# Kernel tuning notes

Hardware: AMD Instinct MI355X
Metric: run time of the kernel (lower is better)

Reference implementation:

```python
import jax, jax.numpy as jnp
import numpy as np

L, N, EMB, H = 4, 50000, 128, 4
R, HID, LBL = 16, 64, 32
E = 625000


def setup_inputs() -> dict:
    key = jax.random.key(0)
    ks = jax.random.split(key, 10)
    s = 0.05
    return {
        "embedding": jax.random.normal(ks[0], (L, N, EMB), jnp.float32),
        "in_proj_w": jax.random.normal(ks[1], (3 * EMB, EMB), jnp.float32) * s,
        "in_proj_b": jnp.zeros((3 * EMB,), jnp.float32),
        "out_proj_w": jax.random.normal(ks[2], (EMB, EMB), jnp.float32) * s,
        "out_proj_b": jnp.zeros((EMB,), jnp.float32),
        "w1": jax.random.normal(ks[3], (R, EMB, HID), jnp.float32) * s,
        "root1": jax.random.normal(ks[4], (EMB, HID), jnp.float32) * s,
        "b1": jnp.zeros((HID,), jnp.float32),
        "w2": jax.random.normal(ks[5], (R, HID, LBL), jnp.float32) * s,
        "root2": jax.random.normal(ks[6], (HID, LBL), jnp.float32) * s,
        "b2": jnp.zeros((LBL,), jnp.float32),
        "edge_index": jax.random.randint(ks[7], (2, E), 0, N, dtype=jnp.int64),
        "edge_type": jax.random.randint(ks[8], (E,), 0, R, dtype=jnp.int64),
    }


def mha_self(x, wi, bi, wo, bo):
    # x: (L, N, EMB) -- torch nn.MultiheadAttention, batch_first=False, q=k=v=x
    Ls, Ns, Es = x.shape
    hd = Es // H
    qkv = x @ wi.T + bi                      # (L, N, 3E)
    q, k, v = jnp.split(qkv, 3, axis=-1)
    q = q.reshape(Ls, Ns, H, hd)
    k = k.reshape(Ls, Ns, H, hd)
    v = v.reshape(Ls, Ns, H, hd)
    scores = jnp.einsum('lnhd,mnhd->nhlm', q, k) / np.sqrt(hd).astype(np.float32)
    attn = jax.nn.softmax(scores, axis=-1)
    out = jnp.einsum('nhlm,mnhd->lnhd', attn, v).reshape(Ls, Ns, Es)
    return out @ wo.T + bo


def rgcn_layer(x, src, dst, etype, W, root, bias):
    # PyG RGCNConv (num_bases=None, aggr='mean'):
    # out[n] = x[n] @ root + bias + sum_r mean_{e: dst=n, type=r} x[src_e] @ W[r]
    Rr, fin, fout = W.shape
    seg = etype * N + dst                                   # (E,) combined (rel, dst)
    msg_sum = jax.ops.segment_sum(x[src], seg, num_segments=Rr * N)   # (R*N, fin)
    cnt = jax.ops.segment_sum(jnp.ones((src.shape[0],), x.dtype), seg,
                              num_segments=Rr * N)
    mean = (msg_sum / jnp.maximum(cnt, 1.0)[:, None]).reshape(Rr, N, fin)
    agg = jnp.einsum('rni,rio->no', mean, W)                # per-relation GEMM
    return agg + x @ root + bias


def reference(embedding, in_proj_w, in_proj_b, out_proj_w, out_proj_b,
              w1, root1, b1, w2, root2, b2, edge_index, edge_type):
    attn_out = mha_self(embedding, in_proj_w, in_proj_b, out_proj_w, out_proj_b)
    x = attn_out[0]                                         # (N, EMB)
    src, dst = edge_index[0], edge_index[1]
    x = jax.nn.relu(rgcn_layer(x, src, dst, edge_type, w1, root1, b1))
    x = rgcn_layer(x, src, dst, edge_type, w2, root2, b2)
    return jax.nn.softmax(x, axis=-1)
```

## Files before the change

kernel.cpp:

```cpp
#include <hip/hip_runtime.h>
#include <hip/hip_bf16.h>
#include <math.h>

#define NNODES 50000
#define NEDGE 625000
#define RREL 16
#define SCAN_NB 196

typedef __attribute__((ext_vector_type(8))) short short8;
typedef __attribute__((ext_vector_type(4))) float f32x4;

__device__ __forceinline__ float bfu(ushort u) {
  return __uint_as_float(((unsigned)u) << 16);
}
__device__ __forceinline__ ushort f2b(float f) {
  __hip_bfloat16 h = __float2bfloat16(f);
  return *(ushort*)&h;
}

__global__ __launch_bounds__(256) void prep_weights(
    const float* __restrict__ ipw, const float* __restrict__ opw,
    const float* __restrict__ w1, const float* __restrict__ root1,
    const float* __restrict__ w2, const float* __restrict__ root2,
    __hip_bfloat16* __restrict__ BTqkv, __hip_bfloat16* __restrict__ BToutT,
    __hip_bfloat16* __restrict__ BT1, __hip_bfloat16* __restrict__ BT2) {
  int i = blockIdx.x * 256 + threadIdx.x;
  if (i < 49152) {
    BTqkv[i] = __float2bfloat16(ipw[i]);
  } else if (i < 65536) {
    int j = i - 49152; int m = j / 128, c = j % 128;
    BToutT[j] = __float2bfloat16(opw[c * 128 + m]);
  } else if (i < 65536 + 139264) {
    int j = i - 65536; int c = j / 128, k = j % 128;
    float v;
    if (c < 64) v = root1[k * 64 + c];
    else { int r = (c - 64) >> 6, o = (c - 64) & 63; v = w1[r * 8192 + k * 64 + o]; }
    BT1[j] = __float2bfloat16(v);
  } else if (i < 65536 + 139264 + 34816) {
    int j = i - 65536 - 139264; int c = j / 64, k = j % 64;
    float v;
    if (c < 32) v = root2[k * 32 + c];
    else { int r = (c - 32) >> 5, o = (c - 32) & 31; v = w2[r * 2048 + k * 32 + o]; }
    BT2[j] = __float2bfloat16(v);
  }
}

__global__ __launch_bounds__(256) void prep_bias1(
    const float* __restrict__ opb, const float* __restrict__ w1,
    const float* __restrict__ root1, float* __restrict__ bias1) {
  int j = blockIdx.x * 256 + threadIdx.x;
  if (j >= 1088) return;
  float s = 0.f;
  if (j < 64) {
    for (int c = 0; c < 128; c++) s += opb[c] * root1[c * 64 + j];
  } else {
    int r = (j - 64) >> 6, o = (j - 64) & 63;
    for (int c = 0; c < 128; c++) s += opb[c] * w1[r * 8192 + c * 64 + o];
  }
  bias1[j] = s;
}

__global__ __launch_bounds__(256) void qkv_gemm(
    const float* __restrict__ A, const __hip_bfloat16* __restrict__ BT,
    const float* __restrict__ bias, __hip_bfloat16* __restrict__ C) {
  __shared__ ushort As[128 * 128];
  __shared__ ushort Cs[128 * 136];
  const int t = threadIdx.x;
  const long row0 = (long)blockIdx.x * 128;

  {
    float4 fa[16];
#pragma unroll
    for (int it = 0; it < 8; it++) {
      int c = t + it * 256;
      int r = c >> 4, cc = c & 15;
      long gm = row0 + r; if (gm > 199999) gm = 199999;
      const float* ap = A + gm * 128 + cc * 8;
      fa[2 * it]     = *(const float4*)ap;
      fa[2 * it + 1] = *(const float4*)(ap + 4);
    }
#pragma unroll
    for (int it = 0; it < 8; it++) {
      int c = t + it * 256;
      int r = c >> 4, cc = c & 15;
      int4 v = make_int4(0, 0, 0, 0);
      if (row0 + r < 200000) {
        float4 f0 = fa[2 * it], f1 = fa[2 * it + 1];
        v.x = (int)f2b(f0.x) | ((int)f2b(f0.y) << 16);
        v.y = (int)f2b(f0.z) | ((int)f2b(f0.w) << 16);
        v.z = (int)f2b(f1.x) | ((int)f2b(f1.y) << 16);
        v.w = (int)f2b(f1.z) | ((int)f2b(f1.w) << 16);
      }
      *(int4*)(As + r * 128 + ((cc ^ (r & 7)) * 8)) = v;
    }
  }
  __syncthreads();

  const int lane = t & 63, w = t >> 6;
  const int wr = (w >> 1) * 64, wc = (w & 1) * 64;
  const int lrow = lane & 15, lk = lane >> 4;
  const int nstrips = (row0 < NNODES) ? 3 : 2;

  for (int s = 0; s < nstrips; s++) {
    const int col0 = (s == 2) ? 0 : 128 + s * 128;
    const long Meff = (s == 2) ? NNODES : 200000;

    const ushort* bp[4];
#pragma unroll
    for (int j = 0; j < 4; j++)
      bp[j] = (const ushort*)BT + (long)(col0 + wc + j * 16 + lrow) * 128 + lk * 8;

    short8 bfr[4][4];
#pragma unroll
    for (int k0 = 0; k0 < 4; k0++)
#pragma unroll
      for (int j = 0; j < 4; j++)
        bfr[k0][j] = *(const short8*)(bp[j] + k0 * 32);

    f32x4 acc[4][4];
#pragma unroll
    for (int i = 0; i < 4; i++)
#pragma unroll
      for (int j = 0; j < 4; j++) acc[i][j] = (f32x4){0.f, 0.f, 0.f, 0.f};

#pragma unroll
    for (int k0 = 0; k0 < 4; k0++) {
      const int cb = k0 * 4 + lk;
      short8 af[4];
#pragma unroll
      for (int i = 0; i < 4; i++) {
        int ra = wr + i * 16 + lrow;
        af[i] = *(const short8*)(As + ra * 128 + ((cb ^ (ra & 7)) * 8));
      }
#pragma unroll
      for (int i = 0; i < 4; i++)
#pragma unroll
        for (int j = 0; j < 4; j++)
          acc[i][j] = __builtin_amdgcn_mfma_f32_16x16x32_bf16(af[i], bfr[k0][j], acc[i][j], 0, 0, 0);
    }

    __syncthreads();
#pragma unroll
    for (int j = 0; j < 4; j++) {
      int coll = wc + j * 16 + lrow;
      float bv = bias[col0 + coll];
#pragma unroll
      for (int i = 0; i < 4; i++) {
        int rbase = wr + i * 16 + lk * 4;
#pragma unroll
        for (int q = 0; q < 4; q++)
          Cs[(rbase + q) * 136 + coll] = f2b(acc[i][j][q] + bv);
      }
    }
    __syncthreads();
#pragma unroll
    for (int idx = t; idx < 128 * 16; idx += 256) {
      int r = idx >> 4, k = idx & 15;
      long gm = row0 + r;
      if (gm < Meff)
        *(int4*)((ushort*)C + gm * 384 + col0 + k * 8) = *(const int4*)(Cs + r * 136 + k * 8);
    }
  }
}

#define EPILOGUE_STORE(MEFF, NCOLS, LDC, BIASEXPR)                              \
  for (int p = 0; p < 2; p++) {                                                 \
    __syncthreads();                                                            \
    if ((w >> 1) == p) {                                                        \
      _Pragma("unroll")                                                         \
      for (int j = 0; j < 4; j++) {                                             \
        int coll = wc + j * 16 + lrow;                                          \
        float bv = (BIASEXPR);                                                  \
        _Pragma("unroll")                                                       \
        for (int i = 0; i < 4; i++) {                                           \
          int rloc = i * 16 + lk * 4;                                           \
          _Pragma("unroll")                                                     \
          for (int q = 0; q < 4; q++)                                           \
            Cs[(rloc + q) * 132 + coll] = f2b(acc[i][j][q] + bv);               \
        }                                                                       \
      }                                                                         \
    }                                                                           \
    __syncthreads();                                                            \
    _Pragma("unroll")                                                           \
    for (int idx = t; idx < 64 * 16; idx += 256) {                              \
      int r = idx >> 4, k = idx & 15;                                           \
      long gm = row0 + p * 64 + r;                                              \
      int col = col0 + k * 8;                                                   \
      if (gm < (MEFF) && col < (NCOLS))                                         \
        *(int4*)((ushort*)C + gm * (LDC) + col) = *(const int4*)(Cs + r * 132 + k * 8); \
    }                                                                           \
  }

template <int K>
__global__ __launch_bounds__(256) void gemm_strips(
    const __hip_bfloat16* __restrict__ Av, const __hip_bfloat16* __restrict__ BT,
    const float* __restrict__ bias, __hip_bfloat16* __restrict__ C,
    int M, int N, int ldc, int spg) {
  constexpr int CPR = K / 8;
  constexpr int NIT = 128 * CPR / 256;
  constexpr int NK0 = K / 32;
  __shared__ ushort As[128 * K];
  __shared__ ushort Cs[64 * 132];
  const int t = threadIdx.x;
  const long row0 = (long)blockIdx.x * 128;

  {
    int4 st[NIT];
#pragma unroll
    for (int it = 0; it < NIT; it++) {
      int c = t + it * 256;
      int r = c / CPR, cc = c % CPR;
      long gm = row0 + r; if (gm > M - 1) gm = M - 1;
      st[it] = *(const int4*)((const ushort*)Av + gm * K + cc * 8);
    }
#pragma unroll
    for (int it = 0; it < NIT; it++) {
      int c = t + it * 256;
      int r = c / CPR, cc = c % CPR;
      int4 v = (row0 + r < M) ? st[it] : make_int4(0, 0, 0, 0);
      *(int4*)(As + r * K + ((cc ^ (r & 7)) * 8)) = v;
    }
  }
  __syncthreads();

  const int lane = t & 63, w = t >> 6;
  const int wr = (w >> 1) * 64, wc = (w & 1) * 64;
  const int lrow = lane & 15, lk = lane >> 4;
  const int nstrips = (N + 127) / 128;
  const int sbeg = blockIdx.y * spg;
  const int send = min(sbeg + spg, nstrips);

  for (int s = sbeg; s < send; s++) {
    const int col0 = s * 128;

    const ushort* bp[4];
#pragma unroll
    for (int j = 0; j < 4; j++) {
      int gn = col0 + wc + j * 16 + lrow;
      if (gn > N - 1) gn = N - 1;
      bp[j] = (const ushort*)BT + (long)gn * K + lk * 8;
    }

    short8 bfr[NK0][4];
#pragma unroll
    for (int k0 = 0; k0 < NK0; k0++)
#pragma unroll
      for (int j = 0; j < 4; j++)
        bfr[k0][j] = *(const short8*)(bp[j] + k0 * 32);

    f32x4 acc[4][4];
#pragma unroll
    for (int i = 0; i < 4; i++)
#pragma unroll
      for (int j = 0; j < 4; j++) acc[i][j] = (f32x4){0.f, 0.f, 0.f, 0.f};

#pragma unroll
    for (int k0 = 0; k0 < NK0; k0++) {
      const int cb = k0 * 4 + lk;
      short8 af[4];
#pragma unroll
      for (int i = 0; i < 4; i++) {
        int ra = wr + i * 16 + lrow;
        af[i] = *(const short8*)(As + ra * K + ((cb ^ (ra & 7)) * 8));
      }
#pragma unroll
      for (int i = 0; i < 4; i++)
#pragma unroll
        for (int j = 0; j < 4; j++)
          acc[i][j] = __builtin_amdgcn_mfma_f32_16x16x32_bf16(af[i], bfr[k0][j], acc[i][j], 0, 0, 0);
    }

    EPILOGUE_STORE(M, N, ldc, bias ? bias[min(col0 + coll, N - 1)] : 0.f)
  }
}

__global__ __launch_bounds__(256) void attn_kernel(
    const __hip_bfloat16* __restrict__ qkv, __hip_bfloat16* __restrict__ o0) {
  int w = threadIdx.x >> 6, lane = threadIdx.x & 63;
  int n = blockIdx.x * 4 + w;
  const ushort* base = (const ushort*)qkv;
  uint qv = *(const uint*)(base + (size_t)n * 384 + lane * 2);
  uint kk[4], vv[4];
#pragma unroll
  for (int m = 0; m < 4; m++) {
    kk[m] = *(const uint*)(base + (size_t)(m * NNODES + n) * 384 + 128 + lane * 2);
    vv[m] = *(const uint*)(base + (size_t)(m * NNODES + n) * 384 + 256 + lane * 2);
  }
  float q0 = bfu(qv & 0xffff), q1 = bfu(qv >> 16);
  float s[4];
#pragma unroll
  for (int m = 0; m < 4; m++) {
    float p = q0 * bfu(kk[m] & 0xffff) + q1 * bfu(kk[m] >> 16);
#pragma unroll
    for (int off = 8; off; off >>= 1) p += __shfl_xor(p, off);
    s[m] = p * 0.17677669529663687f;
  }
  float mx = fmaxf(fmaxf(s[0], s[1]), fmaxf(s[2], s[3]));
  float e[4], sum = 0.f;
#pragma unroll
  for (int m = 0; m < 4; m++) { e[m] = __expf(s[m] - mx); sum += e[m]; }
  float inv = 1.0f / sum;
  float o0f = 0.f, o1f = 0.f;
#pragma unroll
  for (int m = 0; m < 4; m++) {
    float wgt = e[m] * inv;
    o0f += wgt * bfu(vv[m] & 0xffff);
    o1f += wgt * bfu(vv[m] >> 16);
  }
  *(uint*)((ushort*)o0 + (size_t)n * 128 + lane * 2) = (uint)f2b(o0f) | ((uint)f2b(o1f) << 16);
}

__global__ __launch_bounds__(256) void count_edges(
    const int* __restrict__ dst, const int* __restrict__ et, int* __restrict__ cnt) {
  int e = blockIdx.x * 256 + threadIdx.x;
  if (e < NEDGE) atomicAdd(&cnt[et[e] * NNODES + dst[e]], 1);
}

__global__ __launch_bounds__(256) void scan1(
    const int* __restrict__ cnt, int* __restrict__ off, int* __restrict__ part) {
  int t = threadIdx.x, b = blockIdx.x;
  int i = b * 256 + t;
  int v = 0;
  if (i < NNODES) {
#pragma unroll
    for (int r = 0; r < RREL; r++) v += cnt[r * NNODES + i];
  }
  __shared__ int sm[256];
  sm[t] = v;
  __syncthreads();
#pragma unroll
  for (int o = 1; o < 256; o <<= 1) {
    int x = (t >= o) ? sm[t - o] : 0;
    __syncthreads();
    sm[t] += x;
    __syncthreads();
  }
  if (i < NNODES) off[i] = sm[t] - v;
  if (t == 255) part[b] = sm[t];
}

__global__ __launch_bounds__(256) void scan2(int* __restrict__ part) {
  int t = threadIdx.x;
  int v = (t < SCAN_NB) ? part[t] : 0;
  __shared__ int sm[256];
  sm[t] = v;
  __syncthreads();
#pragma unroll
  for (int o = 1; o < 256; o <<= 1) {
    int x = (t >= o) ? sm[t - o] : 0;
    __syncthreads();
    sm[t] += x;
    __syncthreads();
  }
  if (t < SCAN_NB) part[t] = sm[t] - v;
}

__global__ __launch_bounds__(256) void scan3(int* __restrict__ off, const int* __restrict__ part) {
  int i = blockIdx.x * 256 + threadIdx.x;
  if (i < NNODES) off[i] += part[blockIdx.x];
  if (i == 0) off[NNODES] = NEDGE;
}

__global__ __launch_bounds__(256) void scatter_edges(
    const int* __restrict__ src, const int* __restrict__ dst, const int* __restrict__ et,
    const int* __restrict__ cnt, const int* __restrict__ off,
    int* __restrict__ fill, unsigned* __restrict__ sorted, float* __restrict__ scales) {
  int e = blockIdx.x * 256 + threadIdx.x;
  if (e >= NEDGE) return;
  int d = dst[e], r = et[e], s = src[e];
  int pos = off[d] + atomicAdd(&fill[d], 1);
  sorted[pos] = (unsigned)s | ((unsigned)r << 16);
  scales[pos] = 1.0f / (float)cnt[r * NNODES + d];
}

__global__ __launch_bounds__(256) void fused1(
    const int* __restrict__ off, const unsigned* __restrict__ sorted,
    const float* __restrict__ scales, const ushort* __restrict__ Y1,
    const float* __restrict__ b1, __hip_bfloat16* __restrict__ x1b) {
  int w = threadIdx.x >> 6, lane = threadIdx.x & 63;
  int d = blockIdx.x * 4 + w;
  int s0 = off[d], s1 = off[d + 1];
  float a[8];
  a[0] = bfu(Y1[(size_t)d * 1088 + lane]) + b1[lane];
#pragma unroll
  for (int j = 1; j < 8; j++) a[j] = 0.f;
  int i = s0;
  for (; i + 7 < s1; i += 8) {
    unsigned p[8];
    float c[8];
#pragma unroll
    for (int j = 0; j < 8; j++) { p[j] = sorted[i + j]; c[j] = scales[i + j]; }
#pragma unroll
    for (int j = 0; j < 8; j++)
      a[j] += bfu(Y1[(size_t)(p[j] & 0xFFFF) * 1088 + 64 + (p[j] >> 16) * 64 + lane]) * c[j];
  }
  for (; i < s1; i++) {
    unsigned p = sorted[i];
    a[0] += bfu(Y1[(size_t)(p & 0xFFFF) * 1088 + 64 + (p >> 16) * 64 + lane]) * scales[i];
  }
  float acc = ((a[0] + a[1]) + (a[2] + a[3])) + ((a[4] + a[5]) + (a[6] + a[7]));
  x1b[(size_t)d * 64 + lane] = __float2bfloat16(fmaxf(acc, 0.f));
}

__global__ __launch_bounds__(256) void fused2(
    const int* __restrict__ off, const unsigned* __restrict__ sorted,
    const float* __restrict__ scales, const ushort* __restrict__ Y2,
    const float* __restrict__ b2, float* __restrict__ out) {
  int w = threadIdx.x >> 6, lane = threadIdx.x & 63;
  int d = blockIdx.x * 4 + w;
  int j = lane & 31, half = lane >> 5;
  int s0 = off[d], s1 = off[d + 1];
  float a0 = 0.f, a1 = 0.f, a2 = 0.f, a3 = 0.f;
  int i = s0 + half;
  for (; i + 6 < s1; i += 8) {
    unsigned p0 = sorted[i], p1 = sorted[i + 2], p2 = sorted[i + 4], p3 = sorted[i + 6];
    float c0 = scales[i], c1 = scales[i + 2], c2 = scales[i + 4], c3 = scales[i + 6];
    a0 += bfu(Y2[(size_t)(p0 & 0xFFFF) * 544 + 32 + (p0 >> 16) * 32 + j]) * c0;
    a1 += bfu(Y2[(size_t)(p1 & 0xFFFF) * 544 + 32 + (p1 >> 16) * 32 + j]) * c1;
    a2 += bfu(Y2[(size_t)(p2 & 0xFFFF) * 544 + 32 + (p2 >> 16) * 32 + j]) * c2;
    a3 += bfu(Y2[(size_t)(p3 & 0xFFFF) * 544 + 32 + (p3 >> 16) * 32 + j]) * c3;
  }
  for (; i < s1; i += 2) {
    unsigned p = sorted[i];
    a0 += bfu(Y2[(size_t)(p & 0xFFFF) * 544 + 32 + (p >> 16) * 32 + j]) * scales[i];
  }
  float acc = (a0 + a1) + (a2 + a3);
  acc += __shfl_xor(acc, 32);
  float v = acc + bfu(Y2[(size_t)d * 544 + j]) + b2[j];
  float mx = v;
#pragma unroll
  for (int o = 16; o; o >>= 1) mx = fmaxf(mx, __shfl_xor(mx, o));
  float e = __expf(v - mx);
  float sum = e;
#pragma unroll
  for (int o = 16; o; o >>= 1) sum += __shfl_xor(sum, o);
  if (half == 0) out[(size_t)d * 32 + j] = e / sum;
}

extern "C" void kernel_launch(void* const* d_in, const int* in_sizes, int n_in,
                              void* d_out, int out_size, void* d_ws, size_t ws_size,
                              hipStream_t stream) {
  (void)in_sizes; (void)n_in; (void)out_size; (void)ws_size;
  const float* emb   = (const float*)d_in[0];
  const float* ipw   = (const float*)d_in[1];
  const float* ipb   = (const float*)d_in[2];
  const float* opw   = (const float*)d_in[3];
  const float* opb   = (const float*)d_in[4];
  const float* w1    = (const float*)d_in[5];
  const float* root1 = (const float*)d_in[6];
  const float* b1    = (const float*)d_in[7];
  const float* w2    = (const float*)d_in[8];
  const float* root2 = (const float*)d_in[9];
  const float* b2    = (const float*)d_in[10];
  const int*   eidx  = (const int*)d_in[11];
  const int*   etype = (const int*)d_in[12];
  const int* srcp = eidx;
  const int* dstp = eidx + NEDGE;

  unsigned char* ws = (unsigned char*)d_ws;
  size_t off_b = 0;
  auto alloc = [&](size_t bytes) {
    unsigned char* p = ws + off_b;
    off_b += (bytes + 255) & ~(size_t)255;
    return p;
  };

  unsigned char* R = alloc(153600000);
  __hip_bfloat16* qkv = (__hip_bfloat16*)R;
  __hip_bfloat16* Y1  = (__hip_bfloat16*)R;
  __hip_bfloat16* Y2  = (__hip_bfloat16*)R;
  __hip_bfloat16* o0  = (__hip_bfloat16*)alloc(12800000);
  __hip_bfloat16* x1b = (__hip_bfloat16*)alloc(6400000);
  int*            cnt = (int*)alloc(3200000);
  int*            offs = (int*)alloc((NNODES + 1) * 4);
  int*            fill = (int*)alloc(NNODES * 4);
  int*            part = (int*)alloc(SCAN_NB * 4);
  unsigned*       sorted = (unsigned*)alloc(NEDGE * 4);
  float*          scales = (float*)alloc(NEDGE * 4);
  __hip_bfloat16* BTqkv  = (__hip_bfloat16*)alloc(98304);
  __hip_bfloat16* BToutT = (__hip_bfloat16*)alloc(32768);
  __hip_bfloat16* BT1    = (__hip_bfloat16*)alloc(278528);
  __hip_bfloat16* BT2    = (__hip_bfloat16*)alloc(69632);
  __hip_bfloat16* BW     = (__hip_bfloat16*)alloc(278528);
  float*          bias1  = (float*)alloc(4352);

  prep_weights<<<dim3((241664 + 255) / 256), dim3(256), 0, stream>>>(
      ipw, opw, w1, root1, w2, root2, BTqkv, BToutT, BT1, BT2);
  prep_bias1<<<dim3(5), dim3(256), 0, stream>>>(opb, w1, root1, bias1);
  hipMemsetAsync(cnt, 0, (size_t)RREL * NNODES * sizeof(int), stream);
  hipMemsetAsync(fill, 0, (size_t)NNODES * sizeof(int), stream);
  count_edges<<<dim3((NEDGE + 255) / 256), dim3(256), 0, stream>>>(dstp, etype, cnt);
  scan1<<<dim3(SCAN_NB), dim3(256), 0, stream>>>(cnt, offs, part);
  scan2<<<dim3(1), dim3(256), 0, stream>>>(part);
  scan3<<<dim3(SCAN_NB), dim3(256), 0, stream>>>(offs, part);
  scatter_edges<<<dim3((NEDGE + 255) / 256), dim3(256), 0, stream>>>(
      srcp, dstp, etype, cnt, offs, fill, sorted, scales);

  gemm_strips<128><<<dim3(9, 1), dim3(256), 0, stream>>>(
      BT1, BToutT, nullptr, BW, 1088, 128, 128, 1);

  qkv_gemm<<<dim3(1563), dim3(256), 0, stream>>>(emb, BTqkv, ipb, qkv);

  attn_kernel<<<dim3(12500), dim3(256), 0, stream>>>(qkv, o0);

  gemm_strips<128><<<dim3(391, 3), dim3(256), 0, stream>>>(
      o0, BW, bias1, Y1, NNODES, 1088, 1088, 3);

  fused1<<<dim3(NNODES / 4), dim3(256), 0, stream>>>(
      offs, sorted, scales, (const ushort*)Y1, b1, x1b);

  gemm_strips<64><<<dim3(391, 2), dim3(256), 0, stream>>>(
      x1b, BT2, nullptr, Y2, NNODES, 544, 544, 3);

  fused2<<<dim3(NNODES / 4), dim3(256), 0, stream>>>(
      offs, sorted, scales, (const ushort*)Y2, b2, (float*)d_out);
}
```

Baseline: 325.9 us.

## Merge prep kernels with edge counting and vectorize attention loads

Three small launches (weight conversion, bias fold, edge counting) become one kernel that picks its job from the block index, which removes launch overhead and lets the independent pieces run at the same time. The attention kernel now handles four nodes per wavefront, with 16 lanes per node doing 16-byte loads and stores of 8 bf16 values. This shortens the cross-lane reduction to two shuffles and cuts the block count by four. Each lane now keeps more registers live.

Measured after the change: 320.2 us, median of 2. No clear change (-1.8%).

```diff
diff --git a/kernel.cpp b/kernel.cpp
--- a/kernel.cpp
+++ b/kernel.cpp
@@ -18,46 +18,52 @@
   return *(ushort*)&h;
 }
 
-__global__ __launch_bounds__(256) void prep_weights(
+__global__ __launch_bounds__(256) void mega_prep(
     const float* __restrict__ ipw, const float* __restrict__ opw,
     const float* __restrict__ w1, const float* __restrict__ root1,
     const float* __restrict__ w2, const float* __restrict__ root2,
+    const float* __restrict__ opb,
+    const int* __restrict__ dst, const int* __restrict__ et,
     __hip_bfloat16* __restrict__ BTqkv, __hip_bfloat16* __restrict__ BToutT,
-    __hip_bfloat16* __restrict__ BT1, __hip_bfloat16* __restrict__ BT2) {
-  int i = blockIdx.x * 256 + threadIdx.x;
-  if (i < 49152) {
-    BTqkv[i] = __float2bfloat16(ipw[i]);
-  } else if (i < 65536) {
-    int j = i - 49152; int m = j / 128, c = j % 128;
-    BToutT[j] = __float2bfloat16(opw[c * 128 + m]);
-  } else if (i < 65536 + 139264) {
-    int j = i - 65536; int c = j / 128, k = j % 128;
-    float v;
-    if (c < 64) v = root1[k * 64 + c];
-    else { int r = (c - 64) >> 6, o = (c - 64) & 63; v = w1[r * 8192 + k * 64 + o]; }
-    BT1[j] = __float2bfloat16(v);
-  } else if (i < 65536 + 139264 + 34816) {
-    int j = i - 65536 - 139264; int c = j / 64, k = j % 64;
-    float v;
-    if (c < 32) v = root2[k * 32 + c];
-    else { int r = (c - 32) >> 5, o = (c - 32) & 31; v = w2[r * 2048 + k * 32 + o]; }
-    BT2[j] = __float2bfloat16(v);
-  }
-}
-
-__global__ __launch_bounds__(256) void prep_bias1(
-    const float* __restrict__ opb, const float* __restrict__ w1,
-    const float* __restrict__ root1, float* __restrict__ bias1) {
-  int j = blockIdx.x * 256 + threadIdx.x;
-  if (j >= 1088) return;
-  float s = 0.f;
-  if (j < 64) {
-    for (int c = 0; c < 128; c++) s += opb[c] * root1[c * 64 + j];
+    __hip_bfloat16* __restrict__ BT1, __hip_bfloat16* __restrict__ BT2,
+    float* __restrict__ bias1, int* __restrict__ cnt) {
+  int b = blockIdx.x, t = threadIdx.x;
+  if (b < 944) {
+    int i = b * 256 + t;
+    if (i < 49152) {
+      BTqkv[i] = __float2bfloat16(ipw[i]);
+    } else if (i < 65536) {
+      int j = i - 49152; int m = j / 128, c = j % 128;
+      BToutT[j] = __float2bfloat16(opw[c * 128 + m]);
+    } else if (i < 65536 + 139264) {
+      int j = i - 65536; int c = j / 128, k = j % 128;
+      float v;
+      if (c < 64) v = root1[k * 64 + c];
+      else { int r = (c - 64) >> 6, o = (c - 64) & 63; v = w1[r * 8192 + k * 64 + o]; }
+      BT1[j] = __float2bfloat16(v);
+    } else if (i < 65536 + 139264 + 34816) {
+      int j = i - 65536 - 139264; int c = j / 64, k = j % 64;
+      float v;
+      if (c < 32) v = root2[k * 32 + c];
+      else { int r = (c - 32) >> 5, o = (c - 32) & 31; v = w2[r * 2048 + k * 32 + o]; }
+      BT2[j] = __float2bfloat16(v);
+    }
+  } else if (b < 949) {
+    int j = (b - 944) * 256 + t;
+    if (j < 1088) {
+      float s = 0.f;
+      if (j < 64) {
+        for (int c = 0; c < 128; c++) s += opb[c] * root1[c * 64 + j];
+      } else {
+        int r = (j - 64) >> 6, o = (j - 64) & 63;
+        for (int c = 0; c < 128; c++) s += opb[c] * w1[r * 8192 + c * 64 + o];
+      }
+      bias1[j] = s;
+    }
   } else {
-    int r = (j - 64) >> 6, o = (j - 64) & 63;
-    for (int c = 0; c < 128; c++) s += opb[c] * w1[r * 8192 + c * 64 + o];
-  }
-  bias1[j] = s;
+    int e = (b - 949) * 256 + t;
+    if (e < NEDGE) atomicAdd(&cnt[et[e] * NNODES + dst[e]], 1);
+  }
 }
 
 __global__ __launch_bounds__(256) void qkv_gemm(
@@ -277,22 +283,36 @@
 __global__ __launch_bounds__(256) void attn_kernel(
     const __hip_bfloat16* __restrict__ qkv, __hip_bfloat16* __restrict__ o0) {
   int w = threadIdx.x >> 6, lane = threadIdx.x & 63;
-  int n = blockIdx.x * 4 + w;
+  int nl = lane >> 4, cl = lane & 15;
+  long n = (long)blockIdx.x * 16 + w * 4 + nl;
   const ushort* base = (const ushort*)qkv;
-  uint qv = *(const uint*)(base + (size_t)n * 384 + lane * 2);
-  uint kk[4], vv[4];
+  int4 qv = *(const int4*)(base + n * 384 + cl * 8);
+  int4 kq[4], vq[4];
 #pragma unroll
   for (int m = 0; m < 4; m++) {
-    kk[m] = *(const uint*)(base + (size_t)(m * NNODES + n) * 384 + 128 + lane * 2);
-    vv[m] = *(const uint*)(base + (size_t)(m * NNODES + n) * 384 + 256 + lane * 2);
-  }
-  float q0 = bfu(qv & 0xffff), q1 = bfu(qv >> 16);
+    const ushort* p = base + ((long)m * NNODES + n) * 384;
+    kq[m] = *(const int4*)(p + 128 + cl * 8);
+    vq[m] = *(const int4*)(p + 256 + cl * 8);
+  }
+  float qf[8];
+  {
+    const uint* qu = (const uint*)&qv;
+#pragma unroll
+    for (int x = 0; x < 4; x++) {
+      qf[2 * x] = bfu(qu[x] & 0xffff);
+      qf[2 * x + 1] = bfu(qu[x] >> 16);
+    }
+  }
   float s[4];
 #pragma unroll
   for (int m = 0; m < 4; m++) {
-    float p = q0 * bfu(kk[m] & 0xffff) + q1 * bfu(kk[m] >> 16);
-#pragma unroll
-    for (int off = 8; off; off >>= 1) p += __shfl_xor(p, off);
+    const uint* ku = (const uint*)&kq[m];
+    float p = 0.f;
+#pragma unroll
+    for (int x = 0; x < 4; x++)
+      p += qf[2 * x] * bfu(ku[x] & 0xffff) + qf[2 * x + 1] * bfu(ku[x] >> 16);
+    p += __shfl_xor(p, 1);
+    p += __shfl_xor(p, 2);
     s[m] = p * 0.17677669529663687f;
   }
   float mx = fmaxf(fmaxf(s[0], s[1]), fmaxf(s[2], s[3]));
@@ -300,20 +320,23 @@
 #pragma unroll
   for (int m = 0; m < 4; m++) { e[m] = __expf(s[m] - mx); sum += e[m]; }
   float inv = 1.0f / sum;
-  float o0f = 0.f, o1f = 0.f;
+  float o[8] = {0.f, 0.f, 0.f, 0.f, 0.f, 0.f, 0.f, 0.f};
 #pragma unroll
   for (int m = 0; m < 4; m++) {
+    const uint* vu = (const uint*)&vq[m];
     float wgt = e[m] * inv;
-    o0f += wgt * bfu(vv[m] & 0xffff);
-    o1f += wgt * bfu(vv[m] >> 16);
-  }
-  *(uint*)((ushort*)o0 + (size_t)n * 128 + lane * 2) = (uint)f2b(o0f) | ((uint)f2b(o1f) << 16);
-}
-
-__global__ __launch_bounds__(256) void count_edges(
-    const int* __restrict__ dst, const int* __restrict__ et, int* __restrict__ cnt) {
-  int e = blockIdx.x * 256 + threadIdx.x;
-  if (e < NEDGE) atomicAdd(&cnt[et[e] * NNODES + dst[e]], 1);
+#pragma unroll
+    for (int x = 0; x < 4; x++) {
+      o[2 * x]     += wgt * bfu(vu[x] & 0xffff);
+      o[2 * x + 1] += wgt * bfu(vu[x] >> 16);
+    }
+  }
+  int4 ov;
+  uint* ou = (uint*)&ov;
+#pragma unroll
+  for (int x = 0; x < 4; x++)
+    ou[x] = (uint)f2b(o[2 * x]) | ((uint)f2b(o[2 * x + 1]) << 16);
+  *(int4*)((ushort*)o0 + n * 128 + cl * 8) = ov;
 }
 
 __global__ __launch_bounds__(256) void scan1(
@@ -484,12 +507,11 @@
   __hip_bfloat16* BW     = (__hip_bfloat16*)alloc(278528);
   float*          bias1  = (float*)alloc(4352);
 
-  prep_weights<<<dim3((241664 + 255) / 256), dim3(256), 0, stream>>>(
-      ipw, opw, w1, root1, w2, root2, BTqkv, BToutT, BT1, BT2);
-  prep_bias1<<<dim3(5), dim3(256), 0, stream>>>(opb, w1, root1, bias1);
   hipMemsetAsync(cnt, 0, (size_t)RREL * NNODES * sizeof(int), stream);
   hipMemsetAsync(fill, 0, (size_t)NNODES * sizeof(int), stream);
-  count_edges<<<dim3((NEDGE + 255) / 256), dim3(256), 0, stream>>>(dstp, etype, cnt);
+  mega_prep<<<dim3(3391), dim3(256), 0, stream>>>(
+      ipw, opw, w1, root1, w2, root2, opb, dstp, etype,
+      BTqkv, BToutT, BT1, BT2, bias1, cnt);
   scan1<<<dim3(SCAN_NB), dim3(256), 0, stream>>>(cnt, offs, part);
   scan2<<<dim3(1), dim3(256), 0, stream>>>(part);
   scan3<<<dim3(SCAN_NB), dim3(256), 0, stream>>>(offs, part);
@@ -501,7 +523,7 @@
 
   qkv_gemm<<<dim3(1563), dim3(256), 0, stream>>>(emb, BTqkv, ipb, qkv);
 
-  attn_kernel<<<dim3(12500), dim3(256), 0, stream>>>(qkv, o0);
+  attn_kernel<<<dim3(3125), dim3(256), 0, stream>>>(qkv, o0);
 
   gemm_strips<128><<<dim3(391, 3), dim3(256), 0, stream>>>(
       o0, BW, bias1, Y1, NNODES, 1088, 1088, 3);
```
